# Optimization experiments

Hardware: AMD Instinct MI355X
Metric: run time of the kernel (lower is better)

Reference implementation:

```python
import jax, jax.numpy as jnp
import numpy as np

N_NODES = 100000
N_EDGES = 1600000
C_IN = 128
C_OUT = 128


def setup_inputs() -> dict:
    key = jax.random.key(0)
    k1, k2, k3 = jax.random.split(key, 3)
    x = jax.random.normal(k1, (N_NODES, C_IN), dtype=jnp.float32)
    edge_index = jax.random.randint(k2, (2, N_EDGES), 0, N_NODES, dtype=jnp.int64)
    # Linear(in, out, bias=False) weight has shape [out, in]
    W = jax.random.normal(k3, (C_OUT, C_IN), dtype=jnp.float32) * 0.05
    return {"x": x, "edge_index": edge_index, "W": W}


def reference(x, edge_index, W):
    # Original builds dense A (adj[src,dst] += 1 per edge, counting duplicates),
    # adds self-loops I, computes d = A.sum(dim=0) (column sums = in-degree + 1),
    # then out = diag(1/d) @ A @ diag(1/d) @ (x @ W.T).
    # Equivalent edge-wise O(E) form:
    #   out[i] = (1/d[i]) * ( sum_{(i,j) in edges} h[j]/d[j]  +  h[i]/d[i] )
    N = x.shape[0]
    src, dst = edge_index[0], edge_index[1]
    # d[j] = (# edges with dst=j) + 1 (self-loop)
    deg = jax.ops.segment_sum(jnp.ones(src.shape[0], dtype=x.dtype), dst, num_segments=N) + 1.0
    h = x @ W.T                      # [N, C_out]
    hn = h / deg[:, None]            # h[j]/d[j]
    agg = jax.ops.segment_sum(hn[dst], src, num_segments=N) + hn  # neighbor msgs + self-loop
    return agg / deg[:, None]
```

## Files before the change

### kernel.cpp

```cpp
#include <hip/hip_runtime.h>
#include <hip/hip_bf16.h>

#define C 128
#define TPB 256
#define TPB3 1024
#define BWID 512
#define NBUK 256

typedef __attribute__((ext_vector_type(8))) _Float16 half8;
typedef __attribute__((ext_vector_type(4))) float f32x4;
typedef __attribute__((ext_vector_type(2))) float fv2;
typedef __attribute__((ext_vector_type(2))) int iv2;
typedef __attribute__((ext_vector_type(2))) long long ll2;
typedef unsigned long long u64;

#define OFF_FLAG  0x0
#define OFF_BSS   0x400
#define OFF_BSD   0xC00
#define OFF_CSUM  0x1400
#define OFF_HISTS 0x10000
#define OFF_HISTD 0x50000
#define OFF_OFFS  0xA0000
#define OFF_CNTS  0x110000
#define OFF_INVD  0x180000
#define OFF_EDST  0x200000
#define OFF_HN    0x900000

__device__ __forceinline__ unsigned f2bf_bits(float f) {
    unsigned u = __float_as_uint(f);
    return (u + 0x7fffu + ((u >> 16) & 1u)) >> 16;
}

__global__ __launch_bounds__(TPB3) void hist_kernel(const void* __restrict__ edges,
                                                    long long E, int chunk,
                                                    int* __restrict__ src32,
                                                    int* __restrict__ dst32,
                                                    int* __restrict__ histS,
                                                    int* __restrict__ histD,
                                                    int* __restrict__ flagp) {
    __shared__ int flag_s;
    __shared__ int hs[NBUK], hd[NBUK];
    const int t = threadIdx.x;
    const int B = blockIdx.x;
    if (t == 0) flag_s = 0;
    if (t < NBUK) { hs[t] = 0; hd[t] = 0; }
    __syncthreads();
    {
        const unsigned* ew = (const unsigned*)edges;
        int any = 0;
        for (int k = t; k < 2048; k += TPB3) {
            const long long widx = 2LL * k + 1;
            if (widx < 2 * E) any |= (ew[widx] != 0u);
        }
        if (any) atomicOr(&flag_s, 1);
    }
    __syncthreads();
    const int is32 = flag_s;
    if (t == 0) *flagp = is32;
    const int Eeven = ((E & 1) == 0);
    const long long b0 = (long long)B * chunk;
    for (int i = 2 * t; i < chunk; i += 2 * TPB3) {
        const long long e0 = b0 + i;
        const bool v0 = (e0 < E);
        const bool v1 = (i + 1 < chunk) && (e0 + 1 < E);
        int s0 = 0, d0 = 0, s1 = 0, d1 = 0;
        if (is32) {
            const int* p = (const int*)edges;
            if (v0 && v1 && Eeven) {
                const iv2 sv = *(const iv2*)(p + e0);
                const iv2 dv = *(const iv2*)(p + E + e0);
                s0 = sv.x; s1 = sv.y; d0 = dv.x; d1 = dv.y;
            } else {
                if (v0) { s0 = p[e0]; d0 = p[E + e0]; }
                if (v1) { s1 = p[e0 + 1]; d1 = p[E + e0 + 1]; }
            }
        } else {
            const long long* p = (const long long*)edges;
            if (v0 && v1 && Eeven) {
                const ll2 sv = *(const ll2*)(p + e0);
                const ll2 dv = *(const ll2*)(p + E + e0);
                s0 = (int)sv.x; s1 = (int)sv.y; d0 = (int)dv.x; d1 = (int)dv.y;
            } else {
                if (v0) { s0 = (int)p[e0]; d0 = (int)p[E + e0]; }
                if (v1) { s1 = (int)p[e0 + 1]; d1 = (int)p[E + e0 + 1]; }
            }
            if (v0 && v1) {
                *(iv2*)(src32 + e0) = (iv2){s0, s1};
                *(iv2*)(dst32 + e0) = (iv2){d0, d1};
            } else {
                if (v0) { src32[e0] = s0; dst32[e0] = d0; }
                if (v1) { src32[e0 + 1] = s1; dst32[e0 + 1] = d1; }
            }
        }
        if (v0) { atomicAdd(&hs[s0 >> 9], 1); atomicAdd(&hd[d0 >> 9], 1); }
        if (v1) { atomicAdd(&hs[s1 >> 9], 1); atomicAdd(&hd[d1 >> 9], 1); }
    }
    __syncthreads();
    if (t < NBUK) {
        histS[B * NBUK + t] = hs[t];
        histD[B * NBUK + t] = hd[t];
    }
}

__global__ __launch_bounds__(TPB) void colscan_kernel(int* __restrict__ histS,
                                                      int* __restrict__ histD,
                                                      int* __restrict__ csum) {
    __shared__ int s[TPB];
    const int t = threadIdx.x;
    const int which = blockIdx.x >> 8;
    const int b = blockIdx.x & (NBUK - 1);
    int* hist = which ? histD : histS;
    const int v = hist[t * NBUK + b];
    s[t] = v;
    __syncthreads();
    for (int d = 1; d < TPB; d <<= 1) {
        const int a = (t >= d) ? s[t - d] : 0;
        __syncthreads();
        s[t] += a;
        __syncthreads();
    }
    hist[t * NBUK + b] = s[t] - v;
    if (t == TPB - 1) csum[which * NBUK + b] = s[t];
}

__global__ __launch_bounds__(TPB) void bscan_kernel(const int* __restrict__ csum,
                                                    int* __restrict__ bsS,
                                                    int* __restrict__ bsD, int Etot) {
    __shared__ int s[TPB];
    const int t = threadIdx.x;
    int v = csum[t];
    s[t] = v;
    __syncthreads();
    for (int d = 1; d < TPB; d <<= 1) {
        const int a = (t >= d) ? s[t - d] : 0;
        __syncthreads();
        s[t] += a;
        __syncthreads();
    }
    bsS[t] = s[t] - v;
    if (t == TPB - 1) bsS[NBUK] = Etot;
    __syncthreads();
    v = csum[NBUK + t];
    s[t] = v;
    __syncthreads();
    for (int d = 1; d < TPB; d <<= 1) {
        const int a = (t >= d) ? s[t - d] : 0;
        __syncthreads();
        s[t] += a;
        __syncthreads();
    }
    bsD[t] = s[t] - v;
    if (t == TPB - 1) bsD[NBUK] = Etot;
}

__global__ __launch_bounds__(TPB3) void scatter_kernel(const void* __restrict__ edges,
                                                       const int* __restrict__ flagp,
                                                       const int* __restrict__ src32,
                                                       const int* __restrict__ dst32,
                                                       long long E, int chunk,
                                                       const int* __restrict__ histS,
                                                       const int* __restrict__ histD,
                                                       const int* __restrict__ bsS,
                                                       const int* __restrict__ bsD,
                                                       u64* __restrict__ partS,
                                                       int* __restrict__ partD) {
    __shared__ int cs[NBUK], cd[NBUK];
    const int t = threadIdx.x;
    const int B = blockIdx.x;
    if (t < NBUK) {
        cs[t] = histS[B * NBUK + t] + bsS[t];
        cd[t] = histD[B * NBUK + t] + bsD[t];
    }
    __syncthreads();
    const int is32 = *flagp;
    const int* sp = is32 ? (const int*)edges : src32;
    const int* dp = is32 ? (const int*)edges + E : dst32;
    const int Eeven = ((E & 1) == 0);
    const long long b0 = (long long)B * chunk;
    for (int i = 2 * t; i < chunk; i += 2 * TPB3) {
        const long long e0 = b0 + i;
        const bool v0 = (e0 < E);
        const bool v1 = (i + 1 < chunk) && (e0 + 1 < E);
        int s0 = 0, d0 = 0, s1 = 0, d1 = 0;
        if (v0 && v1 && Eeven) {
            const iv2 sv = *(const iv2*)(sp + e0);
            const iv2 dv = *(const iv2*)(dp + e0);
            s0 = sv.x; s1 = sv.y; d0 = dv.x; d1 = dv.y;
        } else {
            if (v0) { s0 = sp[e0]; d0 = dp[e0]; }
            if (v1) { s1 = sp[e0 + 1]; d1 = dp[e0 + 1]; }
        }
        if (v0) {
            const int ps = atomicAdd(&cs[s0 >> 9], 1);
            partS[ps] = ((u64)(unsigned)d0 << 32) | (unsigned)s0;
            const int pd = atomicAdd(&cd[d0 >> 9], 1);
            partD[pd] = d0;
        }
        if (v1) {
            const int ps = atomicAdd(&cs[s1 >> 9], 1);
            partS[ps] = ((u64)(unsigned)d1 << 32) | (unsigned)s1;
            const int pd = atomicAdd(&cd[d1 >> 9], 1);
            partD[pd] = d1;
        }
    }
}

__global__ __launch_bounds__(TPB3) void csrdeg_kernel(const u64* __restrict__ partS,
                                                      const int* __restrict__ partD,
                                                      const int* __restrict__ bsS,
                                                      const int* __restrict__ bsD,
                                                      int* __restrict__ offS,
                                                      int* __restrict__ cntS,
                                                      int* __restrict__ eDst,
                                                      float* __restrict__ invd, int N) {
    __shared__ int cnt[BWID], off[BWID];
    __shared__ int wtot[16];
    const int t = threadIdx.x;
    const int B = blockIdx.x;
    const int lo = B * BWID;
    if (lo >= N) return;
    const int wv = t >> 6, ln = t & 63;
    const int eb = bsS[B], ee = bsS[B + 1];
    if (t < BWID) cnt[t] = 0;
    __syncthreads();
    for (int e = eb + t; e < ee; e += TPB3)
        atomicAdd(&cnt[(int)(partS[e] & 0xffffffffu) - lo], 1);
    __syncthreads();
    const int loc = (t < BWID) ? cnt[t] : 0;
    int v = loc;
#pragma unroll
    for (int d = 1; d < 64; d <<= 1) {
        const int n = __shfl_up(v, d);
        if (ln >= d) v += n;
    }
    if (ln == 63) wtot[wv] = v;
    __syncthreads();
    if (wv == 0) {
        const int wv_ = (ln < 16) ? wtot[ln] : 0;
        int w2 = wv_;
#pragma unroll
        for (int d = 1; d < 16; d <<= 1) {
            const int n = __shfl_up(w2, d);
            if (ln >= d) w2 += n;
        }
        if (ln < 16) wtot[ln] = w2 - wv_;
    }
    __syncthreads();
    const int ex = v - loc + wtot[wv];
    if (t < BWID) {
        off[t] = ex;
        const int node = lo + t;
        if (node < N) { offS[node] = eb + ex; cntS[node] = loc; }
    }
    __syncthreads();
    for (int e = eb + t; e < ee; e += TPB3) {
        const u64 p = partS[e];
        const int sv = (int)(p & 0xffffffffu);
        const int dv = (int)(p >> 32);
        const int pos = atomicAdd(&off[sv - lo], 1);
        eDst[eb + pos] = dv;
    }
    __syncthreads();
    if (t < BWID) cnt[t] = 0;
    __syncthreads();
    const int db = bsD[B], de = bsD[B + 1];
    for (int e = db + t; e < de; e += TPB3)
        atomicAdd(&cnt[partD[e] - lo], 1);
    __syncthreads();
    if (t < BWID) {
        const int node = lo + t;
        if (node < N) invd[node] = 1.0f / (float)(cnt[t] + 1);
    }
}

__global__ __launch_bounds__(TPB) void gemm_mfma_kernel(const float* __restrict__ x,
                                                        const float* __restrict__ W,
                                                        const float* __restrict__ invd,
                                                        unsigned short* __restrict__ hn,
                                                        int N) {
    __shared__ _Float16 Wl[C * C];
    const int t = threadIdx.x;
    const int lane = t & 63;
    const int wid = t >> 6;
    const int lr = lane & 15;
    const int lk = lane >> 4;
    const int m0 = blockIdx.x * 128 + wid * 32;

    {
        const float4* W4 = (const float4*)W;
#pragma unroll
        for (int i = 0; i < 16; ++i) {
            const int g = i * TPB + t;
            const float4 v = W4[g];
            const int row = g >> 5;
            const int c4 = g & 31;
            const int chunk = c4 >> 1;
            const int half = c4 & 1;
            union { _Float16 h[4]; unsigned long long u; } p;
            p.h[0] = (_Float16)v.x; p.h[1] = (_Float16)v.y;
            p.h[2] = (_Float16)v.z; p.h[3] = (_Float16)v.w;
            const int off = row * 256 + ((chunk ^ (row & 7)) << 4) + (half << 3);
            *(unsigned long long*)((char*)Wl + off) = p.u;
        }
    }

    half8 a[2][4];
#pragma unroll
    for (int mb = 0; mb < 2; ++mb) {
        const int row = m0 + mb * 16 + lr;
        const float* xp = x + (size_t)row * C + lk * 8;
#pragma unroll
        for (int ks = 0; ks < 4; ++ks) {
            half8 av;
            if (row < N) {
                const float4 v0 = *(const float4*)(xp + ks * 32);
                const float4 v1 = *(const float4*)(xp + ks * 32 + 4);
                av[0] = (_Float16)v0.x; av[1] = (_Float16)v0.y;
                av[2] = (_Float16)v0.z; av[3] = (_Float16)v0.w;
                av[4] = (_Float16)v1.x; av[5] = (_Float16)v1.y;
                av[6] = (_Float16)v1.z; av[7] = (_Float16)v1.w;
            } else {
                av = (half8)((_Float16)0.f);
            }
            a[mb][ks] = av;
        }
    }
    __syncthreads();

    f32x4 acc[2][8];
#pragma unroll
    for (int mb = 0; mb < 2; ++mb)
#pragma unroll
        for (int nf = 0; nf < 8; ++nf)
            acc[mb][nf] = (f32x4){0.f, 0.f, 0.f, 0.f};

#pragma unroll
    for (int nf = 0; nf < 8; ++nf) {
        const int brow = nf * 16 + lr;
        half8 b[4];
#pragma unroll
        for (int ks = 0; ks < 4; ++ks) {
            const int chunkp = (lk + ks * 4) ^ (lr & 7);
            b[ks] = *(const half8*)((const char*)Wl + brow * 256 + chunkp * 16);
        }
#pragma unroll
        for (int mb = 0; mb < 2; ++mb)
#pragma unroll
            for (int ks = 0; ks < 4; ++ks)
                acc[mb][nf] = __builtin_amdgcn_mfma_f32_16x16x32_f16(
                    a[mb][ks], b[ks], acc[mb][nf], 0, 0, 0);
    }

#pragma unroll
    for (int mb = 0; mb < 2; ++mb) {
#pragma unroll
        for (int r = 0; r < 4; ++r) {
            const int row = m0 + mb * 16 + lk * 4 + r;
            if (row < N) {
                const float idv = invd[row];
                unsigned short* hp = hn + (size_t)row * C + lr;
#pragma unroll
                for (int nf = 0; nf < 8; ++nf)
                    hp[nf * 16] = (unsigned short)f2bf_bits(acc[mb][nf][r] * idv);
            }
        }
    }
}

__global__ __launch_bounds__(TPB) void gather_kernel(const int* __restrict__ offS,
                                                     const int* __restrict__ cntS,
                                                     const int* __restrict__ eDst,
                                                     const uint4* __restrict__ hnb4,
                                                     const float* __restrict__ invd,
                                                     float* __restrict__ out, int N) {
    const int lane = threadIdx.x & 63;
    const int w = (blockIdx.x * TPB + threadIdx.x) >> 6;
    if (w >= N) return;
    const int sub = lane >> 4;
    const int ll  = lane & 15;
    const int beg = offS[w];
    const int cnt = cntS[w];
    const int total = cnt + 1;

    float acc[8];
#pragma unroll
    for (int i = 0; i < 8; ++i) acc[i] = 0.f;

    for (int j0 = 0; j0 < total; j0 += 64) {
        const int m = min(64, total - j0);
        int dl = w;
        if (lane < m && j0 + lane < cnt)
            dl = __builtin_nontemporal_load(&eDst[beg + j0 + lane]);
#pragma unroll 4
        for (int q = 0; q < m; q += 4) {
            const int d = __shfl(dl, q + sub);
            if (q + sub < m) {
                const uint4 v = hnb4[(size_t)d * 16 + ll];
                acc[0] += __uint_as_float(v.x << 16);
                acc[1] += __uint_as_float(v.x & 0xffff0000u);
                acc[2] += __uint_as_float(v.y << 16);
                acc[3] += __uint_as_float(v.y & 0xffff0000u);
                acc[4] += __uint_as_float(v.z << 16);
                acc[5] += __uint_as_float(v.z & 0xffff0000u);
                acc[6] += __uint_as_float(v.w << 16);
                acc[7] += __uint_as_float(v.w & 0xffff0000u);
            }
        }
    }

#pragma unroll
    for (int i = 0; i < 8; ++i) {
        acc[i] += __shfl_xor(acc[i], 16);
        acc[i] += __shfl_xor(acc[i], 32);
    }

    const float s = invd[w];
    fv2 o;
    o.x = acc[sub * 2] * s;
    o.y = acc[sub * 2 + 1] * s;
    fv2* op = (fv2*)(out + (size_t)w * C + ll * 8 + sub * 2);
    __builtin_nontemporal_store(o, op);
}

extern "C" void kernel_launch(void* const* d_in, const int* in_sizes, int n_in,
                              void* d_out, int out_size, void* d_ws, size_t ws_size,
                              hipStream_t stream) {
    const float* x = (const float*)d_in[0];
    const void* edges = d_in[1];
    const float* W = (const float*)d_in[2];
    float* out = (float*)d_out;

    const int N = in_sizes[0] / C;
    const long long E = (long long)in_sizes[1] / 2;

    char* ws = (char*)d_ws;
    int*       flagp = (int*)(ws + OFF_FLAG);
    int*       bsS   = (int*)(ws + OFF_BSS);
    int*       bsD   = (int*)(ws + OFF_BSD);
    int*       csum  = (int*)(ws + OFF_CSUM);
    int*       histS = (int*)(ws + OFF_HISTS);
    int*       histD = (int*)(ws + OFF_HISTD);
    int*       offS  = (int*)(ws + OFF_OFFS);
    int*       cntS  = (int*)(ws + OFF_CNTS);
    float*     invd  = (float*)(ws + OFF_INVD);
    int*       eDst  = (int*)(ws + OFF_EDST);
    unsigned short* hn = (unsigned short*)(ws + OFF_HN);

    int* o32   = (int*)d_out;
    int* src32 = o32;
    int* dst32 = o32 + E;
    u64* partS = (u64*)(o32 + 2 * E);
    int* partD = o32 + 6 * E;

    const int chunk = (int)((E + NBUK - 1) / NBUK);

    hist_kernel<<<NBUK, TPB3, 0, stream>>>(edges, E, chunk, src32, dst32,
                                           histS, histD, flagp);
    colscan_kernel<<<2 * NBUK, TPB, 0, stream>>>(histS, histD, csum);
    bscan_kernel<<<1, TPB, 0, stream>>>(csum, bsS, bsD, (int)E);
    scatter_kernel<<<NBUK, TPB3, 0, stream>>>(edges, flagp, src32, dst32, E, chunk,
                                              histS, histD, bsS, bsD, partS, partD);
    csrdeg_kernel<<<NBUK, TPB3, 0, stream>>>(partS, partD, bsS, bsD,
                                             offS, cntS, eDst, invd, N);

    const int nBlkG = (N + 127) / 128;
    gemm_mfma_kernel<<<nBlkG, TPB, 0, stream>>>(x, W, invd, hn, N);

    const int nBlkA = (N * 64 + TPB - 1) / TPB;
    gather_kernel<<<nBlkA, TPB, 0, stream>>>(offS, cntS, eDst, (const uint4*)hn,
                                             invd, out, N);
}
```

Baseline: 137.8 us.

## Replace histogram+scan bucketing with padded per-bucket atomic cursors in one pass

New measurement: 136.0 us (median of 2 runs). About the same (-1.4%).

```diff
diff --git a/kernel.cpp b/kernel.cpp
--- a/kernel.cpp
+++ b/kernel.cpp
@@ -6,6 +6,7 @@
 #define TPB3 1024
 #define BWID 512
 #define NBUK 256
+#define PADB 9472
 
 typedef __attribute__((ext_vector_type(8))) _Float16 half8;
 typedef __attribute__((ext_vector_type(4))) float f32x4;
@@ -14,32 +15,34 @@
 typedef __attribute__((ext_vector_type(2))) long long ll2;
 typedef unsigned long long u64;
 
-#define OFF_FLAG  0x0
-#define OFF_BSS   0x400
-#define OFF_BSD   0xC00
-#define OFF_CSUM  0x1400
-#define OFF_HISTS 0x10000
-#define OFF_HISTD 0x50000
+#define OFF_CURS  0x400
+#define OFF_CURD  0xC00
 #define OFF_OFFS  0xA0000
 #define OFF_CNTS  0x110000
 #define OFF_INVD  0x180000
 #define OFF_EDST  0x200000
-#define OFF_HN    0x900000
+#define OFF_HN    0xC00000
 
 __device__ __forceinline__ unsigned f2bf_bits(float f) {
     unsigned u = __float_as_uint(f);
     return (u + 0x7fffu + ((u >> 16) & 1u)) >> 16;
 }
 
-__global__ __launch_bounds__(TPB3) void hist_kernel(const void* __restrict__ edges,
-                                                    long long E, int chunk,
-                                                    int* __restrict__ src32,
-                                                    int* __restrict__ dst32,
-                                                    int* __restrict__ histS,
-                                                    int* __restrict__ histD,
-                                                    int* __restrict__ flagp) {
+__global__ void init_kernel(int* __restrict__ gcurS, int* __restrict__ gcurD) {
+    const int t = threadIdx.x;
+    gcurS[t] = t * PADB;
+    gcurD[t] = t * PADB;
+}
+
+__global__ __launch_bounds__(TPB3) void scatter2_kernel(const void* __restrict__ edges,
+                                                        long long E, int chunk,
+                                                        int* __restrict__ gcurS,
+                                                        int* __restrict__ gcurD,
+                                                        u64* __restrict__ partS,
+                                                        int* __restrict__ partD) {
     __shared__ int flag_s;
     __shared__ int hs[NBUK], hd[NBUK];
+    __shared__ int cs[NBUK], cd[NBUK];
     const int t = threadIdx.x;
     const int B = blockIdx.x;
     if (t == 0) flag_s = 0;
@@ -56,9 +59,9 @@
     }
     __syncthreads();
     const int is32 = flag_s;
-    if (t == 0) *flagp = is32;
     const int Eeven = ((E & 1) == 0);
     const long long b0 = (long long)B * chunk;
+
     for (int i = 2 * t; i < chunk; i += 2 * TPB3) {
         const long long e0 = b0 + i;
         const bool v0 = (e0 < E);
@@ -84,111 +87,43 @@
                 if (v0) { s0 = (int)p[e0]; d0 = (int)p[E + e0]; }
                 if (v1) { s1 = (int)p[e0 + 1]; d1 = (int)p[E + e0 + 1]; }
             }
-            if (v0 && v1) {
-                *(iv2*)(src32 + e0) = (iv2){s0, s1};
-                *(iv2*)(dst32 + e0) = (iv2){d0, d1};
-            } else {
-                if (v0) { src32[e0] = s0; dst32[e0] = d0; }
-                if (v1) { src32[e0 + 1] = s1; dst32[e0 + 1] = d1; }
-            }
         }
         if (v0) { atomicAdd(&hs[s0 >> 9], 1); atomicAdd(&hd[d0 >> 9], 1); }
         if (v1) { atomicAdd(&hs[s1 >> 9], 1); atomicAdd(&hd[d1 >> 9], 1); }
     }
     __syncthreads();
+
     if (t < NBUK) {
-        histS[B * NBUK + t] = hs[t];
-        histD[B * NBUK + t] = hd[t];
-    }
-}
-
-__global__ __launch_bounds__(TPB) void colscan_kernel(int* __restrict__ histS,
-                                                      int* __restrict__ histD,
-                                                      int* __restrict__ csum) {
-    __shared__ int s[TPB];
-    const int t = threadIdx.x;
-    const int which = blockIdx.x >> 8;
-    const int b = blockIdx.x & (NBUK - 1);
-    int* hist = which ? histD : histS;
-    const int v = hist[t * NBUK + b];
-    s[t] = v;
-    __syncthreads();
-    for (int d = 1; d < TPB; d <<= 1) {
-        const int a = (t >= d) ? s[t - d] : 0;
-        __syncthreads();
-        s[t] += a;
-        __syncthreads();
-    }
-    hist[t * NBUK + b] = s[t] - v;
-    if (t == TPB - 1) csum[which * NBUK + b] = s[t];
-}
-
-__global__ __launch_bounds__(TPB) void bscan_kernel(const int* __restrict__ csum,
-                                                    int* __restrict__ bsS,
-                                                    int* __restrict__ bsD, int Etot) {
-    __shared__ int s[TPB];
-    const int t = threadIdx.x;
-    int v = csum[t];
-    s[t] = v;
-    __syncthreads();
-    for (int d = 1; d < TPB; d <<= 1) {
-        const int a = (t >= d) ? s[t - d] : 0;
-        __syncthreads();
-        s[t] += a;
-        __syncthreads();
-    }
-    bsS[t] = s[t] - v;
-    if (t == TPB - 1) bsS[NBUK] = Etot;
-    __syncthreads();
-    v = csum[NBUK + t];
-    s[t] = v;
-    __syncthreads();
-    for (int d = 1; d < TPB; d <<= 1) {
-        const int a = (t >= d) ? s[t - d] : 0;
-        __syncthreads();
-        s[t] += a;
-        __syncthreads();
-    }
-    bsD[t] = s[t] - v;
-    if (t == TPB - 1) bsD[NBUK] = Etot;
-}
-
-__global__ __launch_bounds__(TPB3) void scatter_kernel(const void* __restrict__ edges,
-                                                       const int* __restrict__ flagp,
-                                                       const int* __restrict__ src32,
-                                                       const int* __restrict__ dst32,
-                                                       long long E, int chunk,
-                                                       const int* __restrict__ histS,
-                                                       const int* __restrict__ histD,
-                                                       const int* __restrict__ bsS,
-                                                       const int* __restrict__ bsD,
-                                                       u64* __restrict__ partS,
-                                                       int* __restrict__ partD) {
-    __shared__ int cs[NBUK], cd[NBUK];
-    const int t = threadIdx.x;
-    const int B = blockIdx.x;
-    if (t < NBUK) {
-        cs[t] = histS[B * NBUK + t] + bsS[t];
-        cd[t] = histD[B * NBUK + t] + bsD[t];
-    }
-    __syncthreads();
-    const int is32 = *flagp;
-    const int* sp = is32 ? (const int*)edges : src32;
-    const int* dp = is32 ? (const int*)edges + E : dst32;
-    const int Eeven = ((E & 1) == 0);
-    const long long b0 = (long long)B * chunk;
+        cs[t] = atomicAdd(&gcurS[t], hs[t]);
+        cd[t] = atomicAdd(&gcurD[t], hd[t]);
+    }
+    __syncthreads();
+
     for (int i = 2 * t; i < chunk; i += 2 * TPB3) {
         const long long e0 = b0 + i;
         const bool v0 = (e0 < E);
         const bool v1 = (i + 1 < chunk) && (e0 + 1 < E);
         int s0 = 0, d0 = 0, s1 = 0, d1 = 0;
-        if (v0 && v1 && Eeven) {
-            const iv2 sv = *(const iv2*)(sp + e0);
-            const iv2 dv = *(const iv2*)(dp + e0);
-            s0 = sv.x; s1 = sv.y; d0 = dv.x; d1 = dv.y;
+        if (is32) {
+            const int* p = (const int*)edges;
+            if (v0 && v1 && Eeven) {
+                const iv2 sv = *(const iv2*)(p + e0);
+                const iv2 dv = *(const iv2*)(p + E + e0);
+                s0 = sv.x; s1 = sv.y; d0 = dv.x; d1 = dv.y;
+            } else {
+                if (v0) { s0 = p[e0]; d0 = p[E + e0]; }
+                if (v1) { s1 = p[e0 + 1]; d1 = p[E + e0 + 1]; }
+            }
         } else {
-            if (v0) { s0 = sp[e0]; d0 = dp[e0]; }
-            if (v1) { s1 = sp[e0 + 1]; d1 = dp[e0 + 1]; }
+            const long long* p = (const long long*)edges;
+            if (v0 && v1 && Eeven) {
+                const ll2 sv = *(const ll2*)(p + e0);
+                const ll2 dv = *(const ll2*)(p + E + e0);
+                s0 = (int)sv.x; s1 = (int)sv.y; d0 = (int)dv.x; d1 = (int)dv.y;
+            } else {
+                if (v0) { s0 = (int)p[e0]; d0 = (int)p[E + e0]; }
+                if (v1) { s1 = (int)p[e0 + 1]; d1 = (int)p[E + e0 + 1]; }
+            }
         }
         if (v0) {
             const int ps = atomicAdd(&cs[s0 >> 9], 1);
@@ -207,8 +142,8 @@
 
 __global__ __launch_bounds__(TPB3) void csrdeg_kernel(const u64* __restrict__ partS,
                                                       const int* __restrict__ partD,
-                                                      const int* __restrict__ bsS,
-                                                      const int* __restrict__ bsD,
+                                                      const int* __restrict__ gcurS,
+                                                      const int* __restrict__ gcurD,
                                                       int* __restrict__ offS,
                                                       int* __restrict__ cntS,
                                                       int* __restrict__ eDst,
@@ -220,7 +155,7 @@
     const int lo = B * BWID;
     if (lo >= N) return;
     const int wv = t >> 6, ln = t & 63;
-    const int eb = bsS[B], ee = bsS[B + 1];
+    const int eb = B * PADB, ee = gcurS[B];
     if (t < BWID) cnt[t] = 0;
     __syncthreads();
     for (int e = eb + t; e < ee; e += TPB3)
@@ -263,7 +198,7 @@
     __syncthreads();
     if (t < BWID) cnt[t] = 0;
     __syncthreads();
-    const int db = bsD[B], de = bsD[B + 1];
+    const int db = B * PADB, de = gcurD[B];
     for (int e = db + t; e < de; e += TPB3)
         atomicAdd(&cnt[partD[e] - lo], 1);
     __syncthreads();
@@ -434,12 +369,8 @@
     const long long E = (long long)in_sizes[1] / 2;
 
     char* ws = (char*)d_ws;
-    int*       flagp = (int*)(ws + OFF_FLAG);
-    int*       bsS   = (int*)(ws + OFF_BSS);
-    int*       bsD   = (int*)(ws + OFF_BSD);
-    int*       csum  = (int*)(ws + OFF_CSUM);
-    int*       histS = (int*)(ws + OFF_HISTS);
-    int*       histD = (int*)(ws + OFF_HISTD);
+    int*       gcurS = (int*)(ws + OFF_CURS);
+    int*       gcurD = (int*)(ws + OFF_CURD);
     int*       offS  = (int*)(ws + OFF_OFFS);
     int*       cntS  = (int*)(ws + OFF_CNTS);
     float*     invd  = (float*)(ws + OFF_INVD);
@@ -447,20 +378,15 @@
     unsigned short* hn = (unsigned short*)(ws + OFF_HN);
 
     int* o32   = (int*)d_out;
-    int* src32 = o32;
-    int* dst32 = o32 + E;
-    u64* partS = (u64*)(o32 + 2 * E);
-    int* partD = o32 + 6 * E;
+    u64* partS = (u64*)o32;
+    int* partD = o32 + 2 * NBUK * PADB;
 
     const int chunk = (int)((E + NBUK - 1) / NBUK);
 
-    hist_kernel<<<NBUK, TPB3, 0, stream>>>(edges, E, chunk, src32, dst32,
-                                           histS, histD, flagp);
-    colscan_kernel<<<2 * NBUK, TPB, 0, stream>>>(histS, histD, csum);
-    bscan_kernel<<<1, TPB, 0, stream>>>(csum, bsS, bsD, (int)E);
-    scatter_kernel<<<NBUK, TPB3, 0, stream>>>(edges, flagp, src32, dst32, E, chunk,
-                                              histS, histD, bsS, bsD, partS, partD);
-    csrdeg_kernel<<<NBUK, TPB3, 0, stream>>>(partS, partD, bsS, bsD,
+    init_kernel<<<1, NBUK, 0, stream>>>(gcurS, gcurD);
+    scatter2_kernel<<<NBUK, TPB3, 0, stream>>>(edges, E, chunk, gcurS, gcurD,
+                                               partS, partD);
+    csrdeg_kernel<<<NBUK, TPB3, 0, stream>>>(partS, partD, gcurS, gcurD,
                                              offS, cntS, eDst, invd, N);
 
     const int nBlkG = (N + 127) / 128;
```
